# Optimization experiments

Hardware: AMD Instinct MI355X
Metric: run time of the kernel (lower is better)

The kernel has to match this reference:

```python
import jax, jax.numpy as jnp
import numpy as np

B = 16384          # graphs (batch)
MAX_NODES = 20     # max nodes per graph
D = 64             # node_embed_dim
DM = 128           # d_model
H = 8              # num_heads
DH = DM // H       # depth per head
SD = 64            # state_embed_dim
N = B * MAX_NODES  # total node rows


def setup_inputs() -> dict:
    key = jax.random.key(0)
    ks = jax.random.split(key, 10)
    node_embed = jax.random.normal(ks[0], (N, D), jnp.float32)
    start_idx = jax.random.randint(ks[1], (B,), 0, N)
    end_idx = jax.random.randint(ks[2], (B,), 0, N)
    # graph id of each node row (agg_state_param = per-graph sum)
    seg_ids = jnp.arange(N, dtype=jnp.int32) // MAX_NODES
    # slots are padding (sparse matmul yields zero rows there) -> idx = -1
    valid = jax.random.uniform(ks[3], (N,)) > 0.2
    pad_idx = jnp.where(valid, jnp.arange(N, dtype=jnp.int32), -1)
    s = 0.05
    Wq = jax.random.normal(ks[4], (3 * D, DM), jnp.float32) * s
    Wk = jax.random.normal(ks[5], (D, DM), jnp.float32) * s
    Wv = jax.random.normal(ks[6], (D, DM), jnp.float32) * s
    Wo = jax.random.normal(ks[7], (DM, SD), jnp.float32) * s
    bq = jnp.zeros((DM,), jnp.float32)
    bk = jnp.zeros((DM,), jnp.float32)
    bv = jnp.zeros((DM,), jnp.float32)
    bo = jnp.zeros((SD,), jnp.float32)
    return {"node_embed": node_embed, "start_idx": start_idx, "end_idx": end_idx,
            "seg_ids": seg_ids, "pad_idx": pad_idx,
            "Wq": Wq, "bq": bq, "Wk": Wk, "bk": bk,
            "Wv": Wv, "bv": bv, "Wo": Wo, "bo": bo}


def reference(node_embed, start_idx, end_idx, seg_ids, pad_idx,
              Wq, bq, Wk, bk, Wv, bv, Wo, bo):
    # sparse one-hot selections -> gathers
    start = node_embed[start_idx]                                  # [B, D]
    end = node_embed[end_idx]                                      # [B, D]
    # agg_state_param -> per-graph sum (segment reduce)
    agg = jax.ops.segment_sum(node_embed, seg_ids, num_segments=B)  # [B, D]
    raw = jnp.concatenate([agg, start, end], axis=1)               # [B, 3D]
    # dropout is identity at inference (training=False)

    # pad_node_param -> gather with zero rows for padded slots
    ok = (pad_idx >= 0)
    nodes = jnp.where(ok[:, None],
                      node_embed[jnp.clip(pad_idx, 0)], 0.0)
    nodes = nodes.reshape(B, MAX_NODES, D)                          # [B, M, D]

    # create_padding_mask: rows whose embedding sums to 0 are padding
    mask = (jnp.sum(nodes, -1) == 0).astype(nodes.dtype)            # [B, M]
    mask = mask[:, None, None, :]                                   # [B,1,1,M]

    q = (raw @ Wq + bq).reshape(B, H, 1, DH)                        # [B,H,1,dh]
    k = (nodes @ Wk + bk).reshape(B, MAX_NODES, H, DH).transpose(0, 2, 1, 3)
    v = (nodes @ Wv + bv).reshape(B, MAX_NODES, H, DH).transpose(0, 2, 1, 3)

    scale = 1.0 / jnp.sqrt(jnp.float32(DH))
    scores = jnp.einsum('bhqd,bhkd->bhqk', q, k) * scale + mask * (-1e9)
    attn = jax.nn.softmax(scores, axis=-1)                          # [B,H,1,M]
    ctx = jnp.einsum('bhqk,bhkd->bhqd', attn, v)                    # [B,H,1,dh]
    ctx = ctx.transpose(0, 2, 1, 3).reshape(B, DM)                  # [B, DM]
    return ctx @ Wo + bo                                            # [B, SD]
```

## Files before the change

kernel.cpp:

```cpp
#include <hip/hip_runtime.h>

#define MAXN 20
#define DD 64
#define DM 128
#define NH 8
#define DH 16
#define SD 64
#define NB 4
#define NROW (NB*MAXN)
#define QKPAD 68

typedef float f32x4 __attribute__((ext_vector_type(4)));
typedef float f32x2 __attribute__((ext_vector_type(2)));

__device__ __forceinline__ int nswz(int row, int q) {
    return (row << 6) + (((q) ^ (row & 15)) << 2);
}

__global__ __launch_bounds__(256) void mha_state_encoder(
    const float* __restrict__ node_embed,
    const int*   __restrict__ start_idx,
    const int*   __restrict__ end_idx,
    const int*   __restrict__ pad_idx,
    const float* __restrict__ Wq, const float* __restrict__ bq,
    const float* __restrict__ Wk, const float* __restrict__ bk,
    const float* __restrict__ Wv, const float* __restrict__ bv,
    const float* __restrict__ Wo, const float* __restrict__ bo,
    float* __restrict__ out)
{
    const int b0 = blockIdx.x * NB;
    const int t  = threadIdx.x;

    __shared__ __align__(16) float nodes[NROW * DD];
    __shared__ __align__(16) float pool[32 * QKPAD];
    __shared__ __align__(16) float pool2[768];
    __shared__ float validf[NROW];

    const float* nbase = node_embed + (size_t)b0 * (MAXN * DD);

    {
        int v = t;
        #pragma unroll
        for (int k2 = 0; k2 < 5; k2++, v += 256) {
            const int row = v >> 4, q = v & 15;
            *(f32x4*)&nodes[nswz(row, q)] = *(const f32x4*)&nbase[(row << 6) + (q << 2)];
        }
    }
    if (t < NROW) validf[t] = (pad_idx[b0 * MAXN + t] >= 0) ? 1.0f : 0.0f;
    {
        const int bb = t >> 6, c = t & 63;
        const float* pg = nbase + bb * (MAXN * DD) + c;
        float s = 0.0f;
        for (int n = 0; n < MAXN; n++) s += pg[n * DD];
        pool2[bb * 192 + c] = s;
        const int rs = start_idx[b0 + bb], re = end_idx[b0 + bb];
        pool2[bb * 192 + DD + c]     = node_embed[(size_t)rs * DD + c];
        pool2[bb * 192 + 2 * DD + c] = node_embed[(size_t)re * DD + c];
    }
    __syncthreads();

    {
        const int jj = (t & 63) * 2;
        const int sg = t >> 6;
        const int i0 = sg * 48;
        f32x2 a0 = {0.f, 0.f}, a1 = a0, a2 = a0, a3 = a0;
        for (int i = 0; i < 48; i++) {
            const f32x2 wv = *(const f32x2*)&Wq[(i0 + i) * DM + jj];
            a0 += wv * pool2[0 * 192 + i0 + i];
            a1 += wv * pool2[1 * 192 + i0 + i];
            a2 += wv * pool2[2 * 192 + i0 + i];
            a3 += wv * pool2[3 * 192 + i0 + i];
        }
        *(f32x2*)&pool[(sg * NB + 0) * DM + jj] = a0;
        *(f32x2*)&pool[(sg * NB + 1) * DM + jj] = a1;
        *(f32x2*)&pool[(sg * NB + 2) * DM + jj] = a2;
        *(f32x2*)&pool[(sg * NB + 3) * DM + jj] = a3;
    }
    __syncthreads();

    {
        const int bb = t >> 7, c = t & 127;
        pool2[bb * DM + c] = bq[c]
            + pool[(0 * NB + bb) * DM + c] + pool[(1 * NB + bb) * DM + c]
            + pool[(2 * NB + bb) * DM + c] + pool[(3 * NB + bb) * DM + c];
        const int o2 = t + 256;
        const int bb2 = o2 >> 7, c2 = o2 & 127;
        pool2[bb2 * DM + c2] = bq[c2]
            + pool[(0 * NB + bb2) * DM + c2] + pool[(1 * NB + bb2) * DM + c2]
            + pool[(2 * NB + bb2) * DM + c2] + pool[(3 * NB + bb2) * DM + c2];
    }
    __syncthreads();

    #pragma unroll
    for (int pr = 0; pr < 2; pr++) {
        const int pp = t + pr * 256;
        const int h = pp >> 6, i = pp & 63;
        const float* wr = &Wk[i * DM + h * DH];
        const f32x4 w0 = *(const f32x4*)&wr[0];
        const f32x4 w1 = *(const f32x4*)&wr[4];
        const f32x4 w2 = *(const f32x4*)&wr[8];
        const f32x4 w3 = *(const f32x4*)&wr[12];
        #pragma unroll
        for (int bb = 0; bb < NB; bb++) {
            const float* qh = &pool2[bb * DM + h * DH];
            const f32x4 q0 = *(const f32x4*)&qh[0];
            const f32x4 q1 = *(const f32x4*)&qh[4];
            const f32x4 q2 = *(const f32x4*)&qh[8];
            const f32x4 q3 = *(const f32x4*)&qh[12];
            const float s =
                  w0[0]*q0[0] + w0[1]*q0[1] + w0[2]*q0[2] + w0[3]*q0[3]
                + w1[0]*q1[0] + w1[1]*q1[1] + w1[2]*q1[2] + w1[3]*q1[3]
                + w2[0]*q2[0] + w2[1]*q2[1] + w2[2]*q2[2] + w2[3]*q2[3]
                + w3[0]*q3[0] + w3[1]*q3[1] + w3[2]*q3[2] + w3[3]*q3[3];
            pool[(bb * NH + h) * QKPAD + i] = s;
        }
    }
    if (t < NB * NH) {
        const int bb = t >> 3, h = t & 7;
        const float* qh  = &pool2[bb * DM + h * DH];
        const float* bkh = &bk[h * DH];
        float s = 0.0f;
        #pragma unroll
        for (int d = 0; d < DH; d++) s += qh[d] * bkh[d];
        pool2[640 + t] = s;
    }
    __syncthreads();

    {
        const int g = t >> 3;
        const int lane8 = t & 7;
        const int bb = g >> 3;
        const float qbv = pool2[640 + g];
        const int qoff = g * QKPAD;
        const int r0 = bb * MAXN + lane8;
        const int r1 = r0 + 8;
        const int r2 = bb * MAXN + 16 + (lane8 & 3);
        const int B0 = r0 << 6, R0 = r0 & 15;
        const int B1 = r1 << 6, R1 = r1 & 15;
        const int B2 = r2 << 6, R2 = r2 & 15;
        float s0 = 0.f, s1 = 0.f, s2 = 0.f;
        #pragma unroll
        for (int c = 0; c < 16; c++) {
            const f32x4 qk4 = *(const f32x4*)&pool[qoff + c * 4];
            const f32x4 n0  = *(const f32x4*)&nodes[B0 + ((c ^ R0) << 2)];
            const f32x4 n1  = *(const f32x4*)&nodes[B1 + ((c ^ R1) << 2)];
            const f32x4 n2  = *(const f32x4*)&nodes[B2 + ((c ^ R2) << 2)];
            s0 += qk4[0]*n0[0] + qk4[1]*n0[1] + qk4[2]*n0[2] + qk4[3]*n0[3];
            s1 += qk4[0]*n1[0] + qk4[1]*n1[1] + qk4[2]*n1[2] + qk4[3]*n1[3];
            s2 += qk4[0]*n2[0] + qk4[1]*n2[1] + qk4[2]*n2[2] + qk4[3]*n2[3];
        }
        float v0 = (s0 + qbv) * 0.25f;
        float v1 = (s1 + qbv) * 0.25f;
        float v2 = (s2 + qbv) * 0.25f;
        if (validf[r0] == 0.0f) v0 -= 1.0e9f;
        if (validf[r1] == 0.0f) v1 -= 1.0e9f;
        pool2[g * MAXN + lane8]     = v0;
        pool2[g * MAXN + 8 + lane8] = v1;
        if (lane8 < 4) {
            if (validf[r2] == 0.0f) v2 -= 1.0e9f;
            pool2[g * MAXN + 16 + lane8] = v2;
        }
    }
    __syncthreads();

    if (t < NB * NH) {
        float m = -INFINITY;
        for (int n = 0; n < MAXN; n++) m = fmaxf(m, pool2[t * MAXN + n]);
        float sum = 0.0f;
        for (int n = 0; n < MAXN; n++) {
            const float e = __expf(pool2[t * MAXN + n] - m);
            pool2[t * MAXN + n] = e;
            sum += e;
        }
        const float inv = 1.0f / sum;
        for (int n = 0; n < MAXN; n++) pool2[t * MAXN + n] *= inv;
    }
    __syncthreads();

    {
        const int g = t >> 3, L = t & 7;
        const int bb = g >> 3;
        f32x4 acc0 = {0.f, 0.f, 0.f, 0.f}, acc1 = acc0;
        for (int n = 0; n < MAXN; n++) {
            const float a = pool2[g * MAXN + n];
            const int row = bb * MAXN + n;
            const int base = row << 6, R = row & 15;
            acc0 += a * *(const f32x4*)&nodes[base + (((2*L)     ^ R) << 2)];
            acc1 += a * *(const f32x4*)&nodes[base + (((2*L + 1) ^ R) << 2)];
        }
        *(f32x4*)&pool[g * QKPAD + L * 8]     = acc0;
        *(f32x4*)&pool[g * QKPAD + L * 8 + 4] = acc1;
    }
    __syncthreads();

    {
        const int j = t & 127, bbp = t >> 7;
        const int h = j >> 4;
        float a0 = bv[j], a1 = a0;
        for (int i = 0; i < DD; i++) {
            const float wv = Wv[i * DM + j];
            a0 += wv * pool[((bbp    ) * NH + h) * QKPAD + i];
            a1 += wv * pool[((bbp + 2) * NH + h) * QKPAD + i];
        }
        pool2[ bbp      * DM + j] = a0;
        pool2[(bbp + 2) * DM + j] = a1;
    }
    __syncthreads();

    {
        const int j = t & 63, sg = t >> 6;
        const int i0 = sg * 32;
        float a0 = 0.f, a1 = 0.f, a2 = 0.f, a3 = 0.f;
        for (int i = 0; i < 32; i++) {
            const float wo = Wo[(i0 + i) * SD + j];
            a0 += wo * pool2[0 * DM + i0 + i];
            a1 += wo * pool2[1 * DM + i0 + i];
            a2 += wo * pool2[2 * DM + i0 + i];
            a3 += wo * pool2[3 * DM + i0 + i];
        }
        pool[(sg * NB + 0) * SD + j] = a0;
        pool[(sg * NB + 1) * SD + j] = a1;
        pool[(sg * NB + 2) * SD + j] = a2;
        pool[(sg * NB + 3) * SD + j] = a3;
    }
    __syncthreads();

    {
        const int bb = t >> 6, j = t & 63;
        const float s = bo[j]
            + pool[(0 * NB + bb) * SD + j] + pool[(1 * NB + bb) * SD + j]
            + pool[(2 * NB + bb) * SD + j] + pool[(3 * NB + bb) * SD + j];
        out[(size_t)(b0 + bb) * SD + j] = s;
    }
}

extern "C" void kernel_launch(void* const* d_in, const int* in_sizes, int n_in,
                              void* d_out, int out_size, void* d_ws, size_t ws_size,
                              hipStream_t stream) {
    const float* node_embed = (const float*)d_in[0];
    const int*   start_idx  = (const int*)d_in[1];
    const int*   end_idx    = (const int*)d_in[2];
    const int*   pad_idx    = (const int*)d_in[4];
    const float* Wq = (const float*)d_in[5];
    const float* bq = (const float*)d_in[6];
    const float* Wk = (const float*)d_in[7];
    const float* bk = (const float*)d_in[8];
    const float* Wv = (const float*)d_in[9];
    const float* bv = (const float*)d_in[10];
    const float* Wo = (const float*)d_in[11];
    const float* bo = (const float*)d_in[12];
    float* out = (float*)d_out;

    mha_state_encoder<<<16384 / NB, 256, 0, stream>>>(
        node_embed, start_idx, end_idx, pad_idx,
        Wq, bq, Wk, bk, Wv, bv, Wo, bo, out);
}
```

Before: 204.5 us.

## Fuse softmax into score stage with warp shuffles and vectorize LDS reads

Softmax over each (graph, head) group is now computed by the 8 lanes that produce the scores, using sub-wavefront shuffle reductions for max and sum. This removes two block barriers and a serial 32-thread softmax phase, and the attn*V accumulation runs in the same phase. The matvec loops for Q, Wv and Wo now read their shared-memory operand as float4 chunks, and the bq reduction uses float2. One risk is that the attention weights are written to shared memory and read back by other lanes of the same 8-lane group without a barrier, which relies on wavefront lockstep.

```diff
diff --git a/kernel.cpp b/kernel.cpp
--- a/kernel.cpp
+++ b/kernel.cpp
@@ -12,10 +12,6 @@
 
 typedef float f32x4 __attribute__((ext_vector_type(4)));
 typedef float f32x2 __attribute__((ext_vector_type(2)));
-
-__device__ __forceinline__ int nswz(int row, int q) {
-    return (row << 6) + (((q) ^ (row & 15)) << 2);
-}
 
 __global__ __launch_bounds__(256) void mha_state_encoder(
     const float* __restrict__ node_embed,
@@ -43,7 +39,8 @@
         #pragma unroll
         for (int k2 = 0; k2 < 5; k2++, v += 256) {
             const int row = v >> 4, q = v & 15;
-            *(f32x4*)&nodes[nswz(row, q)] = *(const f32x4*)&nbase[(row << 6) + (q << 2)];
+            *(f32x4*)&nodes[(row << 6) + ((q ^ (row & 15)) << 2)] =
+                *(const f32x4*)&nbase[(row << 6) + (q << 2)];
         }
     }
     if (t < NROW) validf[t] = (pad_idx[b0 * MAXN + t] >= 0) ? 1.0f : 0.0f;
@@ -64,12 +61,20 @@
         const int sg = t >> 6;
         const int i0 = sg * 48;
         f32x2 a0 = {0.f, 0.f}, a1 = a0, a2 = a0, a3 = a0;
-        for (int i = 0; i < 48; i++) {
-            const f32x2 wv = *(const f32x2*)&Wq[(i0 + i) * DM + jj];
-            a0 += wv * pool2[0 * 192 + i0 + i];
-            a1 += wv * pool2[1 * 192 + i0 + i];
-            a2 += wv * pool2[2 * 192 + i0 + i];
-            a3 += wv * pool2[3 * 192 + i0 + i];
+        for (int c = 0; c < 12; c++) {
+            const int ib = i0 + c * 4;
+            const f32x4 r0 = *(const f32x4*)&pool2[0 * 192 + ib];
+            const f32x4 r1 = *(const f32x4*)&pool2[1 * 192 + ib];
+            const f32x4 r2 = *(const f32x4*)&pool2[2 * 192 + ib];
+            const f32x4 r3 = *(const f32x4*)&pool2[3 * 192 + ib];
+            #pragma unroll
+            for (int u = 0; u < 4; u++) {
+                const f32x2 wv = *(const f32x2*)&Wq[(ib + u) * DM + jj];
+                a0 += wv * r0[u];
+                a1 += wv * r1[u];
+                a2 += wv * r2[u];
+                a3 += wv * r3[u];
+            }
         }
         *(f32x2*)&pool[(sg * NB + 0) * DM + jj] = a0;
         *(f32x2*)&pool[(sg * NB + 1) * DM + jj] = a1;
@@ -79,15 +84,12 @@
     __syncthreads();
 
     {
-        const int bb = t >> 7, c = t & 127;
-        pool2[bb * DM + c] = bq[c]
-            + pool[(0 * NB + bb) * DM + c] + pool[(1 * NB + bb) * DM + c]
-            + pool[(2 * NB + bb) * DM + c] + pool[(3 * NB + bb) * DM + c];
-        const int o2 = t + 256;
-        const int bb2 = o2 >> 7, c2 = o2 & 127;
-        pool2[bb2 * DM + c2] = bq[c2]
-            + pool[(0 * NB + bb2) * DM + c2] + pool[(1 * NB + bb2) * DM + c2]
-            + pool[(2 * NB + bb2) * DM + c2] + pool[(3 * NB + bb2) * DM + c2];
+        const int bb = t >> 6, c2 = (t & 63) * 2;
+        f32x2 s = *(const f32x2*)&bq[c2];
+        #pragma unroll
+        for (int sg = 0; sg < 4; sg++)
+            s += *(const f32x2*)&pool[(sg * NB + bb) * DM + c2];
+        *(f32x2*)&pool2[bb * DM + c2] = s;
     }
     __syncthreads();
 
@@ -138,69 +140,67 @@
         const int B0 = r0 << 6, R0 = r0 & 15;
         const int B1 = r1 << 6, R1 = r1 & 15;
         const int B2 = r2 << 6, R2 = r2 & 15;
-        float s0 = 0.f, s1 = 0.f, s2 = 0.f;
+
+        f32x4 A0 = {0.f, 0.f, 0.f, 0.f}, A1 = A0, A2 = A0;
         #pragma unroll
         for (int c = 0; c < 16; c++) {
             const f32x4 qk4 = *(const f32x4*)&pool[qoff + c * 4];
-            const f32x4 n0  = *(const f32x4*)&nodes[B0 + ((c ^ R0) << 2)];
-            const f32x4 n1  = *(const f32x4*)&nodes[B1 + ((c ^ R1) << 2)];
-            const f32x4 n2  = *(const f32x4*)&nodes[B2 + ((c ^ R2) << 2)];
-            s0 += qk4[0]*n0[0] + qk4[1]*n0[1] + qk4[2]*n0[2] + qk4[3]*n0[3];
-            s1 += qk4[0]*n1[0] + qk4[1]*n1[1] + qk4[2]*n1[2] + qk4[3]*n1[3];
-            s2 += qk4[0]*n2[0] + qk4[1]*n2[1] + qk4[2]*n2[2] + qk4[3]*n2[3];
-        }
-        float v0 = (s0 + qbv) * 0.25f;
-        float v1 = (s1 + qbv) * 0.25f;
-        float v2 = (s2 + qbv) * 0.25f;
+            A0 += qk4 * *(const f32x4*)&nodes[B0 + ((c ^ R0) << 2)];
+            A1 += qk4 * *(const f32x4*)&nodes[B1 + ((c ^ R1) << 2)];
+            A2 += qk4 * *(const f32x4*)&nodes[B2 + ((c ^ R2) << 2)];
+        }
+        float v0 = (A0[0] + A0[1] + A0[2] + A0[3] + qbv) * 0.25f;
+        float v1 = (A1[0] + A1[1] + A1[2] + A1[3] + qbv) * 0.25f;
+        float v2 = (A2[0] + A2[1] + A2[2] + A2[3] + qbv) * 0.25f;
         if (validf[r0] == 0.0f) v0 -= 1.0e9f;
         if (validf[r1] == 0.0f) v1 -= 1.0e9f;
-        pool2[g * MAXN + lane8]     = v0;
-        pool2[g * MAXN + 8 + lane8] = v1;
-        if (lane8 < 4) {
-            if (validf[r2] == 0.0f) v2 -= 1.0e9f;
-            pool2[g * MAXN + 16 + lane8] = v2;
-        }
-    }
-    __syncthreads();
-
-    if (t < NB * NH) {
-        float m = -INFINITY;
-        for (int n = 0; n < MAXN; n++) m = fmaxf(m, pool2[t * MAXN + n]);
-        float sum = 0.0f;
-        for (int n = 0; n < MAXN; n++) {
-            const float e = __expf(pool2[t * MAXN + n] - m);
-            pool2[t * MAXN + n] = e;
-            sum += e;
-        }
+        if (validf[r2] == 0.0f) v2 -= 1.0e9f;
+
+        const float v2m = (lane8 < 4) ? v2 : -3.0e38f;
+        float m = fmaxf(fmaxf(v0, v1), v2m);
+        m = fmaxf(m, __shfl_xor(m, 1, 8));
+        m = fmaxf(m, __shfl_xor(m, 2, 8));
+        m = fmaxf(m, __shfl_xor(m, 4, 8));
+        const float e0 = __expf(v0 - m);
+        const float e1 = __expf(v1 - m);
+        const float e2 = (lane8 < 4) ? __expf(v2 - m) : 0.0f;
+        float sum = e0 + e1 + e2;
+        sum += __shfl_xor(sum, 1, 8);
+        sum += __shfl_xor(sum, 2, 8);
+        sum += __shfl_xor(sum, 4, 8);
         const float inv = 1.0f / sum;
-        for (int n = 0; n < MAXN; n++) pool2[t * MAXN + n] *= inv;
-    }
-    __syncthreads();
-
-    {
-        const int g = t >> 3, L = t & 7;
-        const int bb = g >> 3;
+        pool2[g * MAXN + lane8]     = e0 * inv;
+        pool2[g * MAXN + 8 + lane8] = e1 * inv;
+        if (lane8 < 4) pool2[g * MAXN + 16 + lane8] = e2 * inv;
+
         f32x4 acc0 = {0.f, 0.f, 0.f, 0.f}, acc1 = acc0;
         for (int n = 0; n < MAXN; n++) {
             const float a = pool2[g * MAXN + n];
             const int row = bb * MAXN + n;
             const int base = row << 6, R = row & 15;
-            acc0 += a * *(const f32x4*)&nodes[base + (((2*L)     ^ R) << 2)];
-            acc1 += a * *(const f32x4*)&nodes[base + (((2*L + 1) ^ R) << 2)];
-        }
-        *(f32x4*)&pool[g * QKPAD + L * 8]     = acc0;
-        *(f32x4*)&pool[g * QKPAD + L * 8 + 4] = acc1;
+            acc0 += a * *(const f32x4*)&nodes[base + (((2 * lane8)     ^ R) << 2)];
+            acc1 += a * *(const f32x4*)&nodes[base + (((2 * lane8 + 1) ^ R) << 2)];
+        }
+        *(f32x4*)&pool[g * QKPAD + lane8 * 8]     = acc0;
+        *(f32x4*)&pool[g * QKPAD + lane8 * 8 + 4] = acc1;
     }
     __syncthreads();
 
     {
         const int j = t & 127, bbp = t >> 7;
         const int h = j >> 4;
+        const int po0 = ( bbp      * NH + h) * QKPAD;
+        const int po1 = ((bbp + 2) * NH + h) * QKPAD;
         float a0 = bv[j], a1 = a0;
-        for (int i = 0; i < DD; i++) {
-            const float wv = Wv[i * DM + j];
-            a0 += wv * pool[((bbp    ) * NH + h) * QKPAD + i];
-            a1 += wv * pool[((bbp + 2) * NH + h) * QKPAD + i];
+        for (int ic = 0; ic < 16; ic++) {
+            const f32x4 p0 = *(const f32x4*)&pool[po0 + ic * 4];
+            const f32x4 p1 = *(const f32x4*)&pool[po1 + ic * 4];
+            #pragma unroll
+            for (int u = 0; u < 4; u++) {
+                const float wv = Wv[(ic * 4 + u) * DM + j];
+                a0 += wv * p0[u];
+                a1 += wv * p1[u];
+            }
         }
         pool2[ bbp      * DM + j] = a0;
         pool2[(bbp + 2) * DM + j] = a1;
@@ -211,12 +211,19 @@
         const int j = t & 63, sg = t >> 6;
         const int i0 = sg * 32;
         float a0 = 0.f, a1 = 0.f, a2 = 0.f, a3 = 0.f;
-        for (int i = 0; i < 32; i++) {
-            const float wo = Wo[(i0 + i) * SD + j];
-            a0 += wo * pool2[0 * DM + i0 + i];
-            a1 += wo * pool2[1 * DM + i0 + i];
-            a2 += wo * pool2[2 * DM + i0 + i];
-            a3 += wo * pool2[3 * DM + i0 + i];
+        for (int ic = 0; ic < 8; ic++) {
+            const f32x4 c0 = *(const f32x4*)&pool2[0 * DM + i0 + ic * 4];
+            const f32x4 c1 = *(const f32x4*)&pool2[1 * DM + i0 + ic * 4];
+            const f32x4 c2 = *(const f32x4*)&pool2[2 * DM + i0 + ic * 4];
+            const f32x4 c3 = *(const f32x4*)&pool2[3 * DM + i0 + ic * 4];
+            #pragma unroll
+            for (int u = 0; u < 4; u++) {
+                const float wo = Wo[(i0 + ic * 4 + u) * SD + j];
+                a0 += wo * c0[u];
+                a1 += wo * c1[u];
+                a2 += wo * c2[u];
+                a3 += wo * c3[u];
+            }
         }
         pool[(sg * NB + 0) * SD + j] = a0;
         pool[(sg * NB + 1) * SD + j] = a1;
```

Result: faster. 196.8 us (-3.8%).
